# Optimization experiments

Measured on AMD Instinct MI355X. Metric: run time of the kernel, lower is better.

Reference implementation:

```python
import jax, jax.numpy as jnp
import numpy as np

NH, NKVH, HD = 32, 8, 128
SCALE = 0.08838834764831845  # 1/sqrt(128)
SEQ, CTX = 1024, 3072       # new chunk tokens, cached context tokens
NSLOTS = 8192               # e.g. 512 blocks * block_size 16, slot-flattened


def setup_inputs() -> dict:
    key = jax.random.key(0)
    ks = jax.random.split(key, 5)
    q = jax.random.normal(ks[0], (SEQ, NH * HD), dtype=jnp.float32)
    k = jax.random.normal(ks[1], (SEQ, NKVH * HD), dtype=jnp.float32)
    v = jax.random.normal(ks[2], (SEQ, NKVH * HD), dtype=jnp.float32)
    k_cache = jax.random.normal(ks[3], (NSLOTS, NKVH, HD), dtype=jnp.float32)
    v_cache = jax.random.normal(ks[4], (NSLOTS, NKVH, HD), dtype=jnp.float32)
    # new chunk is stored right after the context region
    slot_mapping = jnp.arange(SEQ, dtype=jnp.int32) + CTX
    context_slots = jnp.arange(CTX, dtype=jnp.int32)
    return {"q": q, "k": k, "v": v, "k_cache": k_cache, "v_cache": v_cache,
            "slot_mapping": slot_mapping, "context_slots": context_slots}


def reference(q, k, v, k_cache, v_cache, slot_mapping, context_slots):
    seq = q.shape[0]
    ctx = context_slots.shape[0]
    qh = q.reshape(seq, NH, HD)
    kh = k.reshape(seq, NKVH, HD)
    vh = v.reshape(seq, NKVH, HD)

    # store_kv_cache: scatter new chunk k/v into paged cache slots
    kc = k_cache.at[slot_mapping].set(kh)
    vc = v_cache.at[slot_mapping].set(vh)

    # gather cached context, then chunked-prefill attention over [ctx | chunk]
    k_all = jnp.concatenate([kc[context_slots], kh], axis=0)  # [L, nkvh, hd]
    v_all = jnp.concatenate([vc[context_slots], vh], axis=0)  # [L, nkvh, hd]
    L = ctx + seq

    group = NH // NKVH
    qg = qh.reshape(seq, NKVH, group, HD) * SCALE
    scores = jnp.einsum('qkgd,lkd->kgql', qg, k_all)  # [nkvh, group, seq, L]

    # full visibility of cached context, causal within the new chunk
    mask = jnp.arange(L)[None, :] <= (ctx + jnp.arange(seq))[:, None]  # [seq, L]
    scores = jnp.where(mask[None, None], scores, jnp.finfo(scores.dtype).min)
    p = jax.nn.softmax(scores, axis=-1)

    o = jnp.einsum('kgql,lkd->qkgd', p, v_all)  # [seq, nkvh, group, hd]
    return o.reshape(seq, NH * HD)
```

## Files before the change

### kernel.cpp

```cpp
#include <hip/hip_runtime.h>

#define NH 32
#define NKVH 8
#define HD 128
#define GRP 4
#define SCALE 0.08838834764831845f

typedef __attribute__((ext_vector_type(8))) __bf16 bf16x8;
typedef __attribute__((ext_vector_type(4))) float f32x4;
typedef __attribute__((ext_vector_type(8))) unsigned short ushort8;

__device__ inline unsigned short f2bf(float x) {
  unsigned int u = __float_as_uint(x);
  u += 0x7fffu + ((u >> 16) & 1u);
  return (unsigned short)(u >> 16);
}

__device__ inline float dpp_max16(float x) {
  x = fmaxf(x, __int_as_float(__builtin_amdgcn_mov_dpp(__float_as_int(x), 0xB1, 0xF, 0xF, true)));
  x = fmaxf(x, __int_as_float(__builtin_amdgcn_mov_dpp(__float_as_int(x), 0x4E, 0xF, 0xF, true)));
  x = fmaxf(x, __int_as_float(__builtin_amdgcn_mov_dpp(__float_as_int(x), 0x141, 0xF, 0xF, true)));
  x = fmaxf(x, __int_as_float(__builtin_amdgcn_mov_dpp(__float_as_int(x), 0x140, 0xF, 0xF, true)));
  return x;
}
__device__ inline float dpp_sum16(float x) {
  x += __int_as_float(__builtin_amdgcn_mov_dpp(__float_as_int(x), 0xB1, 0xF, 0xF, true));
  x += __int_as_float(__builtin_amdgcn_mov_dpp(__float_as_int(x), 0x4E, 0xF, 0xF, true));
  x += __int_as_float(__builtin_amdgcn_mov_dpp(__float_as_int(x), 0x141, 0xF, 0xF, true));
  x += __int_as_float(__builtin_amdgcn_mov_dpp(__float_as_int(x), 0x140, 0xF, 0xF, true));
  return x;
}

__device__ inline void load_lds16(const unsigned short* g, unsigned short* l) {
  __builtin_amdgcn_global_load_lds((const __attribute__((address_space(1))) unsigned int*)g,
                                   (__attribute__((address_space(3))) unsigned int*)l, 16, 0, 0);
}

#define PSTR 72

__global__ __launch_bounds__(256) void prepass_kernel(
    const float* __restrict__ k, const float* __restrict__ v,
    const float* __restrict__ kc, const float* __restrict__ vc,
    const int* __restrict__ slots,
    unsigned short* __restrict__ Kws, unsigned short* __restrict__ Vws,
    int ctx, int L, int kblocks)
{
  if (blockIdx.x < (unsigned)kblocks) {
    const int idx = blockIdx.x * 256 + threadIdx.x;
    const int L8  = L * 8;
    const int kvh = idx / L8;
    const int r2  = idx - kvh * L8;
    const int l   = r2 >> 3;
    const int c16 = idx & 7;
    const float* src = (l < ctx)
        ? kc + ((size_t)slots[l] * NKVH + kvh) * HD + c16 * 16
        : k + (size_t)(l - ctx) * (NKVH * HD) + kvh * HD + c16 * 16;
    float4 f[4];
#pragma unroll
    for (int i = 0; i < 4; ++i) f[i] = ((const float4*)src)[i];
    unsigned short* tile = Kws + (size_t)kvh * L * HD + (size_t)(l >> 6) * 8192;
    const int r = l & 63;
    const int c0 = (2 * c16) ^ (r & 7);
    const int c1 = (2 * c16 + 1) ^ (r & 7);
    ushort8 w0, w1;
    w0[0]=f2bf(f[0].x); w0[1]=f2bf(f[0].y); w0[2]=f2bf(f[0].z); w0[3]=f2bf(f[0].w);
    w0[4]=f2bf(f[1].x); w0[5]=f2bf(f[1].y); w0[6]=f2bf(f[1].z); w0[7]=f2bf(f[1].w);
    w1[0]=f2bf(f[2].x); w1[1]=f2bf(f[2].y); w1[2]=f2bf(f[2].z); w1[3]=f2bf(f[2].w);
    w1[4]=f2bf(f[3].x); w1[5]=f2bf(f[3].y); w1[6]=f2bf(f[3].z); w1[7]=f2bf(f[3].w);
    *(ushort8*)&tile[r * 128 + c0 * 8] = w0;
    *(ushort8*)&tile[r * 128 + c1 * 8] = w1;
  } else {
    const int idx = (blockIdx.x - kblocks) * 256 + threadIdx.x;
    const int d   = idx & 127;
    const int t2  = idx >> 7;
    const int L16 = L >> 4;
    const int kvh = t2 / L16;
    const int lc  = t2 - kvh * L16;
    const int l0  = lc * 16;
    unsigned short vals[16];
#pragma unroll
    for (int i = 0; i < 16; ++i) {
      const int l = l0 + i;
      const float* sp = (l < ctx)
          ? vc + ((size_t)slots[l] * NKVH + kvh) * HD + d
          : v + (size_t)(l - ctx) * (NKVH * HD) + kvh * HD + d;
      vals[i] = f2bf(*sp);
    }
    unsigned short* tile = Vws + (size_t)kvh * L * HD + (size_t)(l0 >> 6) * 8192;
    const int lt  = l0 & 63;
    const int cl0 = lt >> 3;
    ushort8 w0, w1;
#pragma unroll
    for (int i = 0; i < 8; ++i) { w0[i] = vals[i]; w1[i] = vals[8 + i]; }
    *(ushort8*)&tile[d * 64 + ((cl0 ^ (d & 7)) * 8)] = w0;
    *(ushort8*)&tile[d * 64 + (((cl0 + 1) ^ (d & 7)) * 8)] = w1;
  }
}

__global__ __launch_bounds__(256, 2) void attn_kernel(
    const float* __restrict__ q,
    const unsigned short* __restrict__ Kws, const unsigned short* __restrict__ Vws,
    float* __restrict__ out, int ctx, int L)
{
  __shared__ __align__(16) unsigned short Ks[2][8192];
  __shared__ __align__(16) unsigned short VTs[2][8192];
  __shared__ __align__(16) unsigned short Ps[4 * 16 * PSTR];

  const int bx   = blockIdx.x;
  const int kvh  = bx & 7;
  const int g    = (bx >> 3) & 3;
  const int qb   = bx >> 5;
  const int q0   = qb * 64;
  const int head = kvh * GRP + g;

  const int tid  = threadIdx.x;
  const int wave = tid >> 6;
  const int lane = tid & 63;
  const int col  = lane & 15;
  const int quad = lane >> 4;

  bf16x8 qf[4];
  {
    const float* qp = q + (size_t)(q0 + wave * 16 + col) * (NH * HD) + head * HD;
#pragma unroll
    for (int kt = 0; kt < 4; ++kt) {
      const float4 a = *(const float4*)(qp + kt * 32 + quad * 8);
      const float4 b = *(const float4*)(qp + kt * 32 + quad * 8 + 4);
      union { ushort8 u; bf16x8 h; } w;
      w.u[0]=f2bf(a.x*SCALE); w.u[1]=f2bf(a.y*SCALE); w.u[2]=f2bf(a.z*SCALE); w.u[3]=f2bf(a.w*SCALE);
      w.u[4]=f2bf(b.x*SCALE); w.u[5]=f2bf(b.y*SCALE); w.u[6]=f2bf(b.z*SCALE); w.u[7]=f2bf(b.w*SCALE);
      qf[kt] = w.h;
    }
  }

  f32x4 accO[8];
#pragma unroll
  for (int i = 0; i < 8; ++i) accO[i] = (f32x4){0.f, 0.f, 0.f, 0.f};
  float mrow[4] = {-1e30f, -1e30f, -1e30f, -1e30f};
  float lrow[4] = {0.f, 0.f, 0.f, 0.f};

  const int rowbase = q0 + wave * 16 + quad * 4;
  const size_t kvbase = (size_t)kvh * L * HD;
  const int n_tiles = (ctx + q0 + 64) >> 6;

  auto dma_tile = [&](int t, int b) {
    const unsigned short* kg = Kws + kvbase + (size_t)t * 8192;
    const unsigned short* vg = Vws + kvbase + (size_t)t * 8192;
#pragma unroll
    for (int j = 0; j < 4; ++j) {
      const int ch = wave * 4 + j;
      load_lds16(kg + ch * 512 + lane * 8, &Ks[b][ch * 512]);
      load_lds16(vg + ch * 512 + lane * 8, &VTs[b][ch * 512]);
    }
  };

  dma_tile(0, 0);

  for (int it = 0; it < n_tiles; ++it) {
    __syncthreads();

    if (it + 1 < n_tiles) dma_tile(it + 1, (it + 1) & 1);

    const unsigned short* Kb = Ks[it & 1];
    const unsigned short* Vb = VTs[it & 1];
    const int kb = it << 6;

    f32x4 S[4];
#pragma unroll
    for (int nt = 0; nt < 4; ++nt) S[nt] = (f32x4){0.f, 0.f, 0.f, 0.f};
#pragma unroll
    for (int kt = 0; kt < 4; ++kt)
#pragma unroll
      for (int nt = 0; nt < 4; ++nt) {
        const int row = nt * 16 + col;
        const bf16x8 kf = *(const bf16x8*)&Kb[row * 128 + (((kt * 4 + quad) ^ (row & 7)) << 3)];
        S[nt] = __builtin_amdgcn_mfma_f32_16x16x32_bf16(qf[kt], kf, S[nt], 0, 0, 0);
      }

    if (kb + 63 > ctx + q0 + wave * 16) {
#pragma unroll
      for (int r = 0; r < 4; ++r) {
        const int bound = ctx + rowbase + r;
#pragma unroll
        for (int nt = 0; nt < 4; ++nt) {
          const int l = kb + nt * 16 + col;
          if (l > bound) S[nt][r] = -1e30f;
        }
      }
    }

    float alpha[4];
#pragma unroll
    for (int r = 0; r < 4; ++r) {
      float mx = fmaxf(fmaxf(S[0][r], S[1][r]), fmaxf(S[2][r], S[3][r]));
      mx = dpp_max16(mx);
      const float mnew = fmaxf(mrow[r], mx);
      alpha[r] = __expf(mrow[r] - mnew);
      float rs = 0.f;
#pragma unroll
      for (int nt = 0; nt < 4; ++nt) {
        const float p = __expf(S[nt][r] - mnew);
        S[nt][r] = p;
        rs += p;
      }
      rs = dpp_sum16(rs);
      lrow[r] = lrow[r] * alpha[r] + rs;
      mrow[r] = mnew;
    }
#pragma unroll
    for (int dd = 0; dd < 8; ++dd)
#pragma unroll
      for (int r = 0; r < 4; ++r)
        accO[dd][r] *= alpha[r];

    unsigned short* pw = &Ps[wave * 16 * PSTR];
#pragma unroll
    for (int nt = 0; nt < 4; ++nt)
#pragma unroll
      for (int r = 0; r < 4; ++r)
        pw[(quad * 4 + r) * PSTR + nt * 16 + col] = f2bf(S[nt][r]);
    asm volatile("s_waitcnt lgkmcnt(0)" ::: "memory");

    bf16x8 pf[2];
    pf[0] = *(const bf16x8*)&pw[col * PSTR + quad * 8];
    pf[1] = *(const bf16x8*)&pw[col * PSTR + 32 + quad * 8];

#pragma unroll
    for (int nt = 0; nt < 8; ++nt)
#pragma unroll
      for (int kt = 0; kt < 2; ++kt) {
        const int d = nt * 16 + col;
        const bf16x8 vf = *(const bf16x8*)&Vb[d * 64 + (((kt * 4 + quad) ^ (d & 7)) << 3)];
        accO[nt] = __builtin_amdgcn_mfma_f32_16x16x32_bf16(pf[kt], vf, accO[nt], 0, 0, 0);
      }
  }

  float inv[4];
#pragma unroll
  for (int r = 0; r < 4; ++r) inv[r] = 1.0f / lrow[r];
  float* op = out + head * HD;
#pragma unroll
  for (int r = 0; r < 4; ++r) {
    float* orow = op + (size_t)(rowbase + r) * (NH * HD);
#pragma unroll
    for (int nt = 0; nt < 8; ++nt)
      orow[nt * 16 + col] = accO[nt][r] * inv[r];
  }
}

extern "C" void kernel_launch(void* const* d_in, const int* in_sizes, int n_in,
                              void* d_out, int out_size, void* d_ws, size_t ws_size,
                              hipStream_t stream) {
  const float* q  = (const float*)d_in[0];
  const float* k  = (const float*)d_in[1];
  const float* v  = (const float*)d_in[2];
  const float* kc = (const float*)d_in[3];
  const float* vc = (const float*)d_in[4];
  const int* ctx_slots = (const int*)d_in[6];
  float* out = (float*)d_out;

  const int seq = in_sizes[0] / (NH * HD);
  const int ctx = in_sizes[6];
  const int L   = ctx + seq;

  unsigned short* Kws = (unsigned short*)d_ws;
  unsigned short* Vws = Kws + (size_t)NKVH * L * HD;

  const int kthreads = NKVH * L * (HD / 16);
  const int vthreads = NKVH * (L / 16) * HD;
  const int kblocks  = kthreads / 256;
  const int vblocks  = vthreads / 256;
  prepass_kernel<<<kblocks + vblocks, 256, 0, stream>>>(k, v, kc, vc, ctx_slots,
                                                        Kws, Vws, ctx, L, kblocks);

  const int nblocks = (seq / 64) * GRP * NKVH;
  attn_kernel<<<nblocks, 256, 0, stream>>>(q, Kws, Vws, out, ctx, L);
}
```

Measured before the change: 246.7 us.

## Use exp2 softmax with lazy rescaling, packed bf16 converts, and early V loads

Folds log2(e) into the Q scale so softmax uses the hardware exp2. The running max becomes a single value per wave, and the accumulators are rescaled only when the new max exceeds the old one by more than a threshold. Row sums are kept per lane and reduced once at the end, and all bf16 conversions use the packed v_cvt_pk_bf16_f32 instruction. V fragments are read from LDS before the softmax so those loads overlap with it, and the V prepass permutes its load order to match the new P layout. This cuts per-tile VALU and DPP work at the cost of more registers and a looser, shared max, which risks precision if scores spread widely within a wave.

```diff
diff --git a/kernel.cpp b/kernel.cpp
--- a/kernel.cpp
+++ b/kernel.cpp
@@ -5,15 +5,28 @@
 #define HD 128
 #define GRP 4
 #define SCALE 0.08838834764831845f
+#define LOG2E 1.4426950408889634f
+#define PSTR 72
+#define THR 8.0f
 
 typedef __attribute__((ext_vector_type(8))) __bf16 bf16x8;
 typedef __attribute__((ext_vector_type(4))) float f32x4;
 typedef __attribute__((ext_vector_type(8))) unsigned short ushort8;
 
-__device__ inline unsigned short f2bf(float x) {
-  unsigned int u = __float_as_uint(x);
-  u += 0x7fffu + ((u >> 16) & 1u);
-  return (unsigned short)(u >> 16);
+union U8 { ushort8 u; unsigned int d[4]; bf16x8 h; };
+
+__device__ inline unsigned int cvt_pk_bf16(float lo, float hi) {
+  unsigned int r;
+  asm("v_cvt_pk_bf16_f32 %0, %1, %2" : "=v"(r) : "v"(lo), "v"(hi));
+  return r;
+}
+
+__device__ inline float fast_exp2(float x) {
+#if __has_builtin(__builtin_amdgcn_exp2f)
+  return __builtin_amdgcn_exp2f(x);
+#else
+  return exp2f(x);
+#endif
 }
 
 __device__ inline float dpp_max16(float x) {
@@ -35,8 +48,6 @@
   __builtin_amdgcn_global_load_lds((const __attribute__((address_space(1))) unsigned int*)g,
                                    (__attribute__((address_space(3))) unsigned int*)l, 16, 0, 0);
 }
-
-#define PSTR 72
 
 __global__ __launch_bounds__(256) void prepass_kernel(
     const float* __restrict__ k, const float* __restrict__ v,
@@ -62,13 +73,13 @@
     const int r = l & 63;
     const int c0 = (2 * c16) ^ (r & 7);
     const int c1 = (2 * c16 + 1) ^ (r & 7);
-    ushort8 w0, w1;
-    w0[0]=f2bf(f[0].x); w0[1]=f2bf(f[0].y); w0[2]=f2bf(f[0].z); w0[3]=f2bf(f[0].w);
-    w0[4]=f2bf(f[1].x); w0[5]=f2bf(f[1].y); w0[6]=f2bf(f[1].z); w0[7]=f2bf(f[1].w);
-    w1[0]=f2bf(f[2].x); w1[1]=f2bf(f[2].y); w1[2]=f2bf(f[2].z); w1[3]=f2bf(f[2].w);
-    w1[4]=f2bf(f[3].x); w1[5]=f2bf(f[3].y); w1[6]=f2bf(f[3].z); w1[7]=f2bf(f[3].w);
-    *(ushort8*)&tile[r * 128 + c0 * 8] = w0;
-    *(ushort8*)&tile[r * 128 + c1 * 8] = w1;
+    U8 w0, w1;
+    w0.d[0] = cvt_pk_bf16(f[0].x, f[0].y); w0.d[1] = cvt_pk_bf16(f[0].z, f[0].w);
+    w0.d[2] = cvt_pk_bf16(f[1].x, f[1].y); w0.d[3] = cvt_pk_bf16(f[1].z, f[1].w);
+    w1.d[0] = cvt_pk_bf16(f[2].x, f[2].y); w1.d[1] = cvt_pk_bf16(f[2].z, f[2].w);
+    w1.d[2] = cvt_pk_bf16(f[3].x, f[3].y); w1.d[3] = cvt_pk_bf16(f[3].z, f[3].w);
+    *(ushort8*)&tile[r * 128 + c0 * 8] = w0.u;
+    *(ushort8*)&tile[r * 128 + c1 * 8] = w1.u;
   } else {
     const int idx = (blockIdx.x - kblocks) * 256 + threadIdx.x;
     const int d   = idx & 127;
@@ -77,23 +88,28 @@
     const int kvh = t2 / L16;
     const int lc  = t2 - kvh * L16;
     const int l0  = lc * 16;
-    unsigned short vals[16];
-#pragma unroll
-    for (int i = 0; i < 16; ++i) {
-      const int l = l0 + i;
+    const int lB  = l0 & ~63;
+    const int pc2 = (l0 >> 4) & 3;
+    float vals[16];
+#pragma unroll
+    for (int j = 0; j < 16; ++j) {
+      const int l = lB + ((j & 3) << 4) + pc2 * 4 + (j >> 2);
       const float* sp = (l < ctx)
           ? vc + ((size_t)slots[l] * NKVH + kvh) * HD + d
           : v + (size_t)(l - ctx) * (NKVH * HD) + kvh * HD + d;
-      vals[i] = f2bf(*sp);
+      vals[j] = *sp;
+    }
+    U8 w0, w1;
+#pragma unroll
+    for (int i = 0; i < 4; ++i) {
+      w0.d[i] = cvt_pk_bf16(vals[2 * i],     vals[2 * i + 1]);
+      w1.d[i] = cvt_pk_bf16(vals[8 + 2 * i], vals[9 + 2 * i]);
     }
     unsigned short* tile = Vws + (size_t)kvh * L * HD + (size_t)(l0 >> 6) * 8192;
     const int lt  = l0 & 63;
     const int cl0 = lt >> 3;
-    ushort8 w0, w1;
-#pragma unroll
-    for (int i = 0; i < 8; ++i) { w0[i] = vals[i]; w1[i] = vals[8 + i]; }
-    *(ushort8*)&tile[d * 64 + ((cl0 ^ (d & 7)) * 8)] = w0;
-    *(ushort8*)&tile[d * 64 + (((cl0 + 1) ^ (d & 7)) * 8)] = w1;
+    *(ushort8*)&tile[d * 64 + ((cl0 ^ (d & 7)) * 8)] = w0.u;
+    *(ushort8*)&tile[d * 64 + (((cl0 + 1) ^ (d & 7)) * 8)] = w1.u;
   }
 }
 
@@ -121,14 +137,17 @@
 
   bf16x8 qf[4];
   {
+    const float s2 = SCALE * LOG2E;
     const float* qp = q + (size_t)(q0 + wave * 16 + col) * (NH * HD) + head * HD;
 #pragma unroll
     for (int kt = 0; kt < 4; ++kt) {
       const float4 a = *(const float4*)(qp + kt * 32 + quad * 8);
       const float4 b = *(const float4*)(qp + kt * 32 + quad * 8 + 4);
-      union { ushort8 u; bf16x8 h; } w;
-      w.u[0]=f2bf(a.x*SCALE); w.u[1]=f2bf(a.y*SCALE); w.u[2]=f2bf(a.z*SCALE); w.u[3]=f2bf(a.w*SCALE);
-      w.u[4]=f2bf(b.x*SCALE); w.u[5]=f2bf(b.y*SCALE); w.u[6]=f2bf(b.z*SCALE); w.u[7]=f2bf(b.w*SCALE);
+      U8 w;
+      w.d[0] = cvt_pk_bf16(a.x * s2, a.y * s2);
+      w.d[1] = cvt_pk_bf16(a.z * s2, a.w * s2);
+      w.d[2] = cvt_pk_bf16(b.x * s2, b.y * s2);
+      w.d[3] = cvt_pk_bf16(b.z * s2, b.w * s2);
       qf[kt] = w.h;
     }
   }
@@ -136,7 +155,7 @@
   f32x4 accO[8];
 #pragma unroll
   for (int i = 0; i < 8; ++i) accO[i] = (f32x4){0.f, 0.f, 0.f, 0.f};
-  float mrow[4] = {-1e30f, -1e30f, -1e30f, -1e30f};
+  float mrow = -1e30f;
   float lrow[4] = {0.f, 0.f, 0.f, 0.f};
 
   const int rowbase = q0 + wave * 16 + quad * 4;
@@ -177,6 +196,15 @@
         S[nt] = __builtin_amdgcn_mfma_f32_16x16x32_bf16(qf[kt], kf, S[nt], 0, 0, 0);
       }
 
+    bf16x8 vf[8][2];
+#pragma unroll
+    for (int nt = 0; nt < 8; ++nt) {
+      const int d = nt * 16 + col;
+#pragma unroll
+      for (int kt = 0; kt < 2; ++kt)
+        vf[nt][kt] = *(const bf16x8*)&Vb[d * 64 + (((kt * 4 + quad) ^ (d & 7)) << 3)];
+    }
+
     if (kb + 63 > ctx + q0 + wave * 16) {
 #pragma unroll
       for (int r = 0; r < 4; ++r) {
@@ -189,55 +217,56 @@
       }
     }
 
-    float alpha[4];
+    float M = fmaxf(fmaxf(S[0][0], S[0][1]), fmaxf(S[0][2], S[0][3]));
+    M = fmaxf(M, fmaxf(fmaxf(S[1][0], S[1][1]), fmaxf(S[1][2], S[1][3])));
+    M = fmaxf(M, fmaxf(fmaxf(S[2][0], S[2][1]), fmaxf(S[2][2], S[2][3])));
+    M = fmaxf(M, fmaxf(fmaxf(S[3][0], S[3][1]), fmaxf(S[3][2], S[3][3])));
+    M = dpp_max16(M);
+    if (!__all(M - mrow <= THR)) {
+      const float mnew = fmaxf(mrow, M);
+      const float a = fast_exp2(mrow - mnew);
+      mrow = mnew;
+#pragma unroll
+      for (int r = 0; r < 4; ++r) lrow[r] *= a;
+#pragma unroll
+      for (int dd = 0; dd < 8; ++dd)
+#pragma unroll
+        for (int r = 0; r < 4; ++r) accO[dd][r] *= a;
+    }
+#pragma unroll
+    for (int nt = 0; nt < 4; ++nt)
+#pragma unroll
+      for (int r = 0; r < 4; ++r) {
+        const float p = fast_exp2(S[nt][r] - mrow);
+        S[nt][r] = p;
+        lrow[r] += p;
+      }
+
+    unsigned short* pw = &Ps[wave * 16 * PSTR];
 #pragma unroll
     for (int r = 0; r < 4; ++r) {
-      float mx = fmaxf(fmaxf(S[0][r], S[1][r]), fmaxf(S[2][r], S[3][r]));
-      mx = dpp_max16(mx);
-      const float mnew = fmaxf(mrow[r], mx);
-      alpha[r] = __expf(mrow[r] - mnew);
-      float rs = 0.f;
-#pragma unroll
-      for (int nt = 0; nt < 4; ++nt) {
-        const float p = __expf(S[nt][r] - mnew);
-        S[nt][r] = p;
-        rs += p;
-      }
-      rs = dpp_sum16(rs);
-      lrow[r] = lrow[r] * alpha[r] + rs;
-      mrow[r] = mnew;
-    }
-#pragma unroll
-    for (int dd = 0; dd < 8; ++dd)
-#pragma unroll
-      for (int r = 0; r < 4; ++r)
-        accO[dd][r] *= alpha[r];
-
-    unsigned short* pw = &Ps[wave * 16 * PSTR];
-#pragma unroll
-    for (int nt = 0; nt < 4; ++nt)
-#pragma unroll
-      for (int r = 0; r < 4; ++r)
-        pw[(quad * 4 + r) * PSTR + nt * 16 + col] = f2bf(S[nt][r]);
+      const unsigned long long lo = cvt_pk_bf16(S[0][r], S[1][r]);
+      const unsigned long long hi = cvt_pk_bf16(S[2][r], S[3][r]);
+      *(unsigned long long*)&pw[(quad * 4 + r) * PSTR + col * 4] = lo | (hi << 32);
+    }
     asm volatile("s_waitcnt lgkmcnt(0)" ::: "memory");
 
-    bf16x8 pf[2];
-    pf[0] = *(const bf16x8*)&pw[col * PSTR + quad * 8];
-    pf[1] = *(const bf16x8*)&pw[col * PSTR + 32 + quad * 8];
-
-#pragma unroll
-    for (int nt = 0; nt < 8; ++nt)
-#pragma unroll
-      for (int kt = 0; kt < 2; ++kt) {
-        const int d = nt * 16 + col;
-        const bf16x8 vf = *(const bf16x8*)&Vb[d * 64 + (((kt * 4 + quad) ^ (d & 7)) << 3)];
-        accO[nt] = __builtin_amdgcn_mfma_f32_16x16x32_bf16(pf[kt], vf, accO[nt], 0, 0, 0);
-      }
+    const bf16x8 pf0 = *(const bf16x8*)&pw[col * PSTR + quad * 8];
+    const bf16x8 pf1 = *(const bf16x8*)&pw[col * PSTR + 32 + quad * 8];
+
+#pragma unroll
+    for (int nt = 0; nt < 8; ++nt) {
+      accO[nt] = __builtin_amdgcn_mfma_f32_16x16x32_bf16(pf0, vf[nt][0], accO[nt], 0, 0, 0);
+      accO[nt] = __builtin_amdgcn_mfma_f32_16x16x32_bf16(pf1, vf[nt][1], accO[nt], 0, 0, 0);
+    }
   }
 
   float inv[4];
 #pragma unroll
-  for (int r = 0; r < 4; ++r) inv[r] = 1.0f / lrow[r];
+  for (int r = 0; r < 4; ++r) {
+    lrow[r] = dpp_sum16(lrow[r]);
+    inv[r] = 1.0f / lrow[r];
+  }
   float* op = out + head * HD;
 #pragma unroll
   for (int r = 0; r < 4; ++r) {
```

After: 222.2 us. 1.11x faster.
